# Kernel optimization log

Measured on AMD Instinct MI355X. Metric: run time of the kernel, lower is better.

Reference implementation:

```python
import jax, jax.numpy as jnp
import numpy as np

B, S, D = 16, 512, 2048
NUM_HEADS, NUM_GROUPS = 16, 4
HEAD_DIM = D // NUM_HEADS  # 128
MAX_SEQ_LEN, SHARED_SLOTS = 512, 32
EPS = 1e-6


def _rope_tables(seq_positions):
    # inv_freq over half the head dim, as in the module
    inv_freq = 1.0 / (10000.0 ** (jnp.arange(0, HEAD_DIM, 2, dtype=jnp.float32) / HEAD_DIM))
    freqs = jnp.outer(seq_positions.astype(jnp.float32), inv_freq)  # [S, HEAD_DIM//2]
    return jnp.cos(freqs), jnp.sin(freqs)


def _apply_rope(x, cos, sin):
    # x: [b, s, h, head_dim]; cos/sin: [s, 1, head_dim//2] (broadcast over heads)
    x1, x2 = jnp.split(x, 2, axis=-1)
    real = x1 * cos - x2 * sin
    imag = x1 * sin + x2 * cos
    return jnp.concatenate([real, imag], axis=-1).astype(x.dtype)


def _rmsnorm(x, scale):
    # flax RMSNorm with dtype=float32: compute in fp32
    x = x.astype(jnp.float32)
    ms = jnp.mean(jnp.square(x), axis=-1, keepdims=True)
    return x * jax.lax.rsqrt(ms + EPS) * scale


def setup_inputs() -> dict:
    key = jax.random.key(0)
    ks = jax.random.split(key, 10)
    w = 0.02
    return {
        "x": jax.random.normal(ks[0], (B, S, D), dtype=jnp.float32),
        "wq": jax.random.normal(ks[1], (D, D), dtype=jnp.float32) * w,
        "bq": jnp.zeros((D,), dtype=jnp.float32),
        "wk": jax.random.normal(ks[2], (D, NUM_GROUPS * HEAD_DIM), dtype=jnp.float32) * w,
        "bk": jnp.zeros((NUM_GROUPS * HEAD_DIM,), dtype=jnp.float32),
        "wv": jax.random.normal(ks[3], (D, NUM_GROUPS * HEAD_DIM), dtype=jnp.float32) * w,
        "bv": jnp.zeros((NUM_GROUPS * HEAD_DIM,), dtype=jnp.float32),
        "wo": jax.random.normal(ks[4], (D, D), dtype=jnp.float32) * w,
        "bo": jnp.zeros((D,), dtype=jnp.float32),
        "q_norm_scale": jnp.ones((HEAD_DIM,), dtype=jnp.float32),
        "k_norm_scale": jnp.ones((HEAD_DIM,), dtype=jnp.float32),
    }


def reference(x, wq, bq, wk, bk, wv, bv, wo, bo, q_norm_scale, k_norm_scale):
    b, s, d = x.shape
    rep = NUM_HEADS // NUM_GROUPS
    head_scale = HEAD_DIM ** (-0.5)  # applied once explicitly by the module

    # nnx.Linear(dtype=float16): projections computed in fp16
    xh = x.astype(jnp.float16)
    q = (xh @ wq.astype(jnp.float16) + bq.astype(jnp.float16)).reshape(b, s, NUM_HEADS, HEAD_DIM)
    k = (xh @ wk.astype(jnp.float16) + bk.astype(jnp.float16)).reshape(b, s, NUM_GROUPS, HEAD_DIM)
    v = (xh @ wv.astype(jnp.float16) + bv.astype(jnp.float16)).reshape(b, s, NUM_GROUPS, HEAD_DIM)

    # QK RMSNorm (fp32)
    q = _rmsnorm(q, q_norm_scale)
    k = _rmsnorm(k, k_norm_scale)

    # RoPE (default positions 0..s-1)
    pos = jnp.arange(s)
    cos, sin = _rope_tables(pos)
    cos = cos[:, None, :]
    sin = sin[:, None, :]
    q = _apply_rope(q, cos, sin) * head_scale
    k = _apply_rope(k, cos, sin)

    q = q.astype(jnp.float16)
    k = k.astype(jnp.float16)
    v = v.astype(jnp.float16)

    # GQA without materializing repeated k/v: [b, s, groups, rep, head_dim]
    qg = q.reshape(b, s, NUM_GROUPS, rep, HEAD_DIM)
    # dot_product_attention applies its own 1/sqrt(head_dim) (double-scale, faithful)
    logits = jnp.einsum('btgrh,bsgh->bgrts', qg, k,
                        preferred_element_type=jnp.float32) * head_scale

    causal = pos[:, None] >= pos[None, :]  # [s, s]
    logits = jnp.where(causal[None, None, None, :, :], logits, jnp.finfo(jnp.float32).min)
    probs = jax.nn.softmax(logits, axis=-1).astype(jnp.float16)

    out = jnp.einsum('bgrts,bsgh->btgrh', probs, v)  # [b, s, groups, rep, head_dim]
    out = out.reshape(b, s, d)
    return out @ wo.astype(jnp.float16) + bo.astype(jnp.float16)
```

## Files before the change

kernel.cpp:

```cpp
#include <hip/hip_runtime.h>

#define NB 16
#define NS 512
#define ND 2048
#define NH 16
#define NG 4
#define NHD 128
#define NM (NB * NS)
#define NKD (NG * NHD)
#define NKV 1024
#define HEAD_SCALE 0.08838834764831845f

typedef _Float16 h8 __attribute__((ext_vector_type(8)));
typedef float fx4 __attribute__((ext_vector_type(4)));

__device__ __forceinline__ void gload16(const void* g, void* l) {
  __builtin_amdgcn_global_load_lds(
      (__attribute__((address_space(1))) void*)(unsigned long long)g,
      (__attribute__((address_space(3))) void*)(unsigned long long)l,
      16, 0, 0);
}


__global__ void cvt_x_kernel(const float* __restrict__ in, _Float16* __restrict__ out, int n8) {
  int i = blockIdx.x * 256 + threadIdx.x;
  if (i >= n8) return;
  const fx4* p = (const fx4*)in;
  fx4 a = p[2 * i], b = p[2 * i + 1];
  h8 h;
  h[0] = (_Float16)a[0]; h[1] = (_Float16)a[1]; h[2] = (_Float16)a[2]; h[3] = (_Float16)a[3];
  h[4] = (_Float16)b[0]; h[5] = (_Float16)b[1]; h[6] = (_Float16)b[2]; h[7] = (_Float16)b[3];
  ((h8*)out)[i] = h;
}

__global__ void wtrans_kernel(const float* __restrict__ w, _Float16* __restrict__ wt, int K, int N) {
  __shared__ float t[64][65];
  int n0 = blockIdx.x * 64, k0 = blockIdx.y * 64;
#pragma unroll
  for (int it = 0; it < 16; ++it) {
    int idx = it * 256 + threadIdx.x;
    int r = idx >> 6, c = idx & 63;
    t[r][c] = w[(size_t)(k0 + r) * N + n0 + c];
  }
  __syncthreads();
#pragma unroll
  for (int it = 0; it < 16; ++it) {
    int idx = it * 256 + threadIdx.x;
    int r = idx >> 6, c = idx & 63;
    wt[(size_t)(n0 + r) * K + k0 + c] = (_Float16)t[c][r];
  }
}

__global__ void vtrans_kernel(const _Float16* __restrict__ kv, _Float16* __restrict__ vt) {
  __shared__ _Float16 t[64][72];
  int st = blockIdx.x, dt = blockIdx.y, bg = blockIdx.z;
  int b = bg >> 2, g = bg & 3;
  const _Float16* src = kv + ((size_t)(b * NS + st * 64)) * NKV + NKD + g * NHD + dt * 64;
#pragma unroll
  for (int it = 0; it < 2; ++it) {
    int idx = it * 256 + threadIdx.x;
    int r = idx >> 3, c = (idx & 7) * 8;
    *(h8*)&t[r][c] = *(const h8*)(src + (size_t)r * NKV + c);
  }
  __syncthreads();
  _Float16* dst = vt + ((size_t)bg * NHD + dt * 64) * NS + st * 64;
#pragma unroll
  for (int it = 0; it < 2; ++it) {
    int idx = it * 256 + threadIdx.x;
    int r = idx >> 3, c = (idx & 7) * 8;
    h8 o;
#pragma unroll
    for (int e = 0; e < 8; ++e) o[e] = t[c + e][r];
    *(h8*)(dst + (size_t)r * NS + c) = o;
  }
}

__global__ void rope_tables_kernel(float* __restrict__ cosT, float* __restrict__ sinT) {
  int i = blockIdx.x * 256 + threadIdx.x;
  int s = i >> 6, f = i & 63;
  float inv = exp2f(-(float)f * (13.287712379549449f / 64.0f));
  float a = (float)s * inv;
  cosT[i] = cosf(a);
  sinT[i] = sinf(a);
}

__global__ void norm_rope_kernel(_Float16* __restrict__ X, const float* __restrict__ scale,
                                 const float* __restrict__ cosT, const float* __restrict__ sinT,
                                 int hshift, int rowStride, float outScale) {
  int wid = threadIdx.x >> 6, lane = threadIdx.x & 63;
  int task = blockIdx.x * 4 + wid;
  int row = task >> hshift;
  int head = task & ((1 << hshift) - 1);
  _Float16* p = X + (size_t)row * rowStride + head * NHD;
  float x1 = (float)p[lane], x2 = (float)p[lane + 64];
  float ss = x1 * x1 + x2 * x2;
#pragma unroll
  for (int m = 1; m < 64; m <<= 1) ss += __shfl_xor(ss, m, 64);
  float rn = rsqrtf(ss * (1.0f / 128.0f) + 1e-6f);
  int s = row & (NS - 1);
  float c = cosT[s * 64 + lane], sn = sinT[s * 64 + lane];
  float n1 = x1 * rn * scale[lane], n2 = x2 * rn * scale[64 + lane];
  p[lane] = (_Float16)((n1 * c - n2 * sn) * outScale);
  p[lane + 64] = (_Float16)((n1 * sn + n2 * c) * outScale);
}

__device__ __forceinline__ void st_out(float* p, float v) { *p = v; }
__device__ __forceinline__ void st_out(_Float16* p, float v) { *p = (_Float16)v; }


template <typename OT>
__global__ __launch_bounds__(256, 3) void gemm_bt_kernel(
    const _Float16* __restrict__ A, const _Float16* __restrict__ Bt,
    const float* __restrict__ bias, OT* __restrict__ C, int N, int K) {
  __shared__ alignas(16) _Float16 As[128 * 64];
  __shared__ alignas(16) _Float16 Bs[128 * 64];
  const int tid = threadIdx.x;
  const int lane = tid & 63, wid = tid >> 6;
  const int wr = wid >> 1, wc = wid & 1;
  const int la = lane & 15, lb = (lane >> 4) * 8;
  const int bm = blockIdx.y * 128, bn = blockIdx.x * 128;

  fx4 acc[4][4] = {};

  for (int kt = 0; kt < K; kt += 64) {
    const _Float16* Ag = A + (size_t)bm * K + kt;
    const _Float16* Bg = Bt + (size_t)bn * K + kt;
#pragma unroll
    for (int it = 0; it < 4; ++it) {
      int cb = it * 256 + wid * 64;
      int ca = cb + lane;
      int r = ca >> 3, cc = ca & 7;
      gload16(Ag + (size_t)r * K + cc * 8, &As[cb * 8]);
      gload16(Bg + (size_t)r * K + cc * 8, &Bs[cb * 8]);
    }
    __syncthreads();
#pragma unroll
    for (int kk = 0; kk < 2; ++kk) {
      h8 af[4], bf[4];
#pragma unroll
      for (int m = 0; m < 4; ++m)
        af[m] = *(const h8*)&As[(wr * 64 + m * 16 + la) * 64 + kk * 32 + lb];
#pragma unroll
      for (int n = 0; n < 4; ++n)
        bf[n] = *(const h8*)&Bs[(wc * 64 + n * 16 + la) * 64 + kk * 32 + lb];
#pragma unroll
      for (int m = 0; m < 4; ++m)
#pragma unroll
        for (int n = 0; n < 4; ++n)
          acc[m][n] = __builtin_amdgcn_mfma_f32_16x16x32_f16(af[m], bf[n], acc[m][n], 0, 0, 0);
    }
    __syncthreads();
  }
#pragma unroll
  for (int m = 0; m < 4; ++m) {
    int row0 = bm + wr * 64 + m * 16 + (lane >> 4) * 4;
#pragma unroll
    for (int n = 0; n < 4; ++n) {
      int col = bn + wc * 64 + n * 16 + la;
      float bvv = bias[col];
#pragma unroll
      for (int r = 0; r < 4; ++r)
        st_out(&C[(size_t)(row0 + r) * N + col], acc[m][n][r] + bvv);
    }
  }
}


template <typename OT>
__global__ __launch_bounds__(512, 2) void gemm256_kernel(
    const _Float16* __restrict__ A, const _Float16* __restrict__ Bt,
    const float* __restrict__ bias, OT* __restrict__ C, int N, int K) {
  __shared__ alignas(16) _Float16 As[2][2][256 * 32];
  __shared__ alignas(16) _Float16 Bs[2][2][256 * 32];
  const int tid = threadIdx.x;
  const int lane = tid & 63, w = tid >> 6;
  const int wr = w >> 2, wc = w & 3;
  const int la = lane & 15, lq = lane >> 4;
  const int lin = (blockIdx.x & 7) * 32 + (blockIdx.x >> 3);
  const int nbx = N >> 8;
  const int by = lin / nbx, bx = lin % nbx;
  const int bm = by * 256, bn = bx * 256;
  const int NT = K >> 6;

  fx4 acc[8][4] = {};

  {
    const _Float16* Ag = A + (size_t)bm * K;
    const _Float16* Bg = Bt + (size_t)bn * K;
#pragma unroll
    for (int sh = 0; sh < 2; ++sh) {
#pragma unroll
      for (int i = 0; i < 2; ++i) {
        int cb = i * 512 + w * 64;
        int s = cb + lane;
        int r = s >> 2, c = s & 3;
        gload16(Ag + (size_t)r * K + sh * 32 + ((c ^ ((r >> 1) & 3)) << 3), &As[0][sh][cb * 8]);
      }
#pragma unroll
      for (int i = 0; i < 2; ++i) {
        int cb = i * 512 + w * 64;
        int s = cb + lane;
        int r = s >> 2, c = s & 3;
        gload16(Bg + (size_t)r * K + sh * 32 + ((c ^ ((r >> 1) & 3)) << 3), &Bs[0][sh][cb * 8]);
      }
    }
  }
  asm volatile("s_waitcnt vmcnt(4)" ::: "memory");
  __builtin_amdgcn_s_barrier();

  for (int kt = 0; kt < NT; ++kt) {
    const int cur = kt & 1;
    const int nxt = cur ^ 1;
    const bool more = (kt + 1 < NT);
    const _Float16* Ag = A + (size_t)bm * K + (kt + 1) * 64;
    const _Float16* Bg = Bt + (size_t)bn * K + (kt + 1) * 64;
    h8 bf[4];
#pragma unroll
    for (int ph = 0; ph < 4; ++ph) {
      const int kh = ph >> 1, g = ph & 1;
      h8 af[4];
#pragma unroll
      for (int mi = 0; mi < 4; ++mi) {
        int row = wr * 128 + (g * 4 + mi) * 16 + la;
        af[mi] = *(const h8*)&As[cur][kh][row * 32 + ((lq ^ ((row >> 1) & 3)) << 3)];
      }
      if (g == 0) {
#pragma unroll
        for (int ni = 0; ni < 4; ++ni) {
          int row = wc * 64 + ni * 16 + la;
          bf[ni] = *(const h8*)&Bs[cur][kh][row * 32 + ((lq ^ ((row >> 1) & 3)) << 3)];
        }
      }
      if (more) {
        const int sh = ph >> 1;
        const _Float16* Sg = (ph & 1) ? Bg : Ag;
        _Float16* Ld = (ph & 1) ? &Bs[nxt][sh][0] : &As[nxt][sh][0];
#pragma unroll
        for (int i = 0; i < 2; ++i) {
          int cb = i * 512 + w * 64;
          int s = cb + lane;
          int r = s >> 2, c = s & 3;
          gload16(Sg + (size_t)r * K + sh * 32 + ((c ^ ((r >> 1) & 3)) << 3), Ld + cb * 8);
        }
      }
      if (ph == 1 || ph == 3) {
        if (more) asm volatile("s_waitcnt vmcnt(4)" ::: "memory");
        else      asm volatile("s_waitcnt vmcnt(0)" ::: "memory");
      }
      __builtin_amdgcn_s_barrier();
      asm volatile("s_waitcnt lgkmcnt(0)" ::: "memory");
      __builtin_amdgcn_sched_barrier(0);
      __builtin_amdgcn_s_setprio(1);
#pragma unroll
      for (int mi = 0; mi < 4; ++mi)
#pragma unroll
        for (int ni = 0; ni < 4; ++ni)
          acc[g * 4 + mi][ni] = __builtin_amdgcn_mfma_f32_16x16x32_f16(
              af[mi], bf[ni], acc[g * 4 + mi][ni], 0, 0, 0);
      __builtin_amdgcn_s_setprio(0);
      __builtin_amdgcn_sched_barrier(0);
      __builtin_amdgcn_s_barrier();
    }
  }
#pragma unroll
  for (int mi = 0; mi < 8; ++mi) {
    int row0 = bm + wr * 128 + mi * 16 + lq * 4;
#pragma unroll
    for (int ni = 0; ni < 4; ++ni) {
      int col = bn + wc * 64 + ni * 16 + la;
      float bvv = bias[col];
#pragma unroll
      for (int r = 0; r < 4; ++r)
        st_out(&C[(size_t)(row0 + r) * N + col], acc[mi][ni][r] + bvv);
    }
  }
}


__global__ __launch_bounds__(512, 4) void attn_kernel(
    const _Float16* __restrict__ Q, const _Float16* __restrict__ KV,
    const _Float16* __restrict__ Vt, _Float16* __restrict__ ctx) {
  __shared__ alignas(16) _Float16 Ks[2][64 * 128];
  __shared__ alignas(16) _Float16 Vs[2][128 * 64];
  __shared__ alignas(16) _Float16 Ps[8][16 * 64];

  const int bid = blockIdx.x;
  const int logical = (bid & 7) * 64 + (bid >> 3);
  const int b = logical >> 5;
  const int g = (logical >> 3) & 3;
  const int jp = logical & 7;
  const int j1 = jp, j2 = 15 - jp;

  const int tid = threadIdx.x;
  const int lane = tid & 63, w = tid >> 6;
  const int la = lane & 15, lq = lane >> 4;
  const int h = g * 4 + (w & 3);
  const int rh = w >> 2;

  const _Float16* Vg = Vt + (size_t)(b * NG + g) * NHD * NS;

  auto stage = [&](int buf, int kt) {
    const _Float16* Kg = KV + ((size_t)(b * NS + kt * 64)) * NKV + g * NHD;
#pragma unroll
    for (int it = 0; it < 2; ++it) {
      int cb = it * 512 + w * 64;
      int s = cb + lane;
      int rr = s >> 4, c = s & 15;
      gload16(Kg + (size_t)rr * NKV + ((c ^ (rr & 7)) * 8), &Ks[buf][cb * 8]);
    }
#pragma unroll
    for (int it = 0; it < 2; ++it) {
      int cb = it * 512 + w * 64;
      int s = cb + lane;
      int rr = s >> 3, c = s & 7;
      gload16(Vg + (size_t)rr * NS + kt * 64 + ((c ^ (rr & 7)) * 8), &Vs[buf][cb * 8]);
    }
  };

  const int nt1 = ((j1 * 32 + 31) >> 6) + 1;
  const int nt2 = ((j2 * 32 + 31) >> 6) + 1;
  const int ntotal = nt1 + nt2;

  h8 qf[4];
  fx4 oacc[8];
  float mrun[4], lrun[4];

  stage(0, 0);
  int cur = 0;
  for (int t = 0; t < ntotal; ++t) {
    const bool inA = t < nt1;
    const int j = inA ? j1 : j2;
    const int kt = inA ? t : t - nt1;
    const int ntj = inA ? nt1 : nt2;
    __syncthreads();
    if (t + 1 < ntotal) {
      int nkt = (t + 1 < nt1) ? (t + 1) : (t + 1 - nt1);
      stage(cur ^ 1, nkt);
    }
    if (kt == 0) {
      const _Float16* Qg = Q + ((size_t)(b * NS + j * 32 + rh * 16 + la)) * ND + h * NHD + lq * 8;
#pragma unroll
      for (int kc = 0; kc < 4; ++kc) qf[kc] = *(const h8*)(Qg + kc * 32);
#pragma unroll
      for (int f = 0; f < 8; ++f) oacc[f] = fx4{0.f, 0.f, 0.f, 0.f};
#pragma unroll
      for (int r = 0; r < 4; ++r) { mrun[r] = -1e30f; lrun[r] = 0.f; }
    }

    fx4 sc[4] = {};
    __builtin_amdgcn_s_setprio(1);
#pragma unroll
    for (int n = 0; n < 4; ++n) {
      int row = n * 16 + la;
#pragma unroll
      for (int kc = 0; kc < 4; ++kc) {
        h8 bk = *(const h8*)&Ks[cur][row * 128 + (((kc * 4 + lq) ^ (la & 7)) * 8)];
        sc[n] = __builtin_amdgcn_mfma_f32_16x16x32_f16(qf[kc], bk, sc[n], 0, 0, 0);
      }
    }
    __builtin_amdgcn_s_setprio(0);

    const int qrow0 = j * 32 + rh * 16 + lq * 4;
    const bool maskT = (kt == ntj - 1);
    float pv[4][4];
    float rm[4] = {-1e30f, -1e30f, -1e30f, -1e30f};
#pragma unroll
    for (int n = 0; n < 4; ++n) {
      int kv = kt * 64 + n * 16 + la;
#pragma unroll
      for (int r = 0; r < 4; ++r) {
        float sv = sc[n][r] * HEAD_SCALE;
        sv = (maskT && kv > qrow0 + r) ? -1e30f : sv;
        pv[n][r] = sv;
        rm[r] = fmaxf(rm[r], sv);
      }
    }
#pragma unroll
    for (int r = 0; r < 4; ++r) {
#pragma unroll
      for (int m = 1; m < 16; m <<= 1) rm[r] = fmaxf(rm[r], __shfl_xor(rm[r], m, 64));
      float mn = fmaxf(mrun[r], rm[r]);
      float corr = __expf(mrun[r] - mn);
      mrun[r] = mn;
      lrun[r] *= corr;
#pragma unroll
      for (int f = 0; f < 8; ++f) oacc[f][r] *= corr;
    }
    float rs[4] = {0.f, 0.f, 0.f, 0.f};
#pragma unroll
    for (int n = 0; n < 4; ++n)
#pragma unroll
      for (int r = 0; r < 4; ++r) {
        float e = __expf(pv[n][r] - mrun[r]);
        pv[n][r] = e;
        rs[r] += e;
      }
#pragma unroll
    for (int r = 0; r < 4; ++r) {
#pragma unroll
      for (int m = 1; m < 16; m <<= 1) rs[r] += __shfl_xor(rs[r], m, 64);
      lrun[r] += rs[r];
    }

#pragma unroll
    for (int n = 0; n < 4; ++n)
#pragma unroll
      for (int r = 0; r < 4; ++r) {
        int row = lq * 4 + r;
        int chsw = (n * 2 + (la >> 3)) ^ (row & 7);
        Ps[w][row * 64 + chsw * 8 + (la & 7)] = (_Float16)pv[n][r];
      }
    asm volatile("s_waitcnt lgkmcnt(0)" ::: "memory");
    __builtin_amdgcn_sched_barrier(0);
    h8 pf[2];
#pragma unroll
    for (int ks = 0; ks < 2; ++ks)
      pf[ks] = *(const h8*)&Ps[w][la * 64 + (((ks * 4 + lq) ^ (la & 7)) * 8)];

    __builtin_amdgcn_s_setprio(1);
#pragma unroll
    for (int f = 0; f < 8; ++f) {
      int row = f * 16 + la;
#pragma unroll
      for (int ks = 0; ks < 2; ++ks) {
        h8 bv = *(const h8*)&Vs[cur][row * 64 + (((ks * 4 + lq) ^ (la & 7)) * 8)];
        oacc[f] = __builtin_amdgcn_mfma_f32_16x16x32_f16(pf[ks], bv, oacc[f], 0, 0, 0);
      }
    }
    __builtin_amdgcn_s_setprio(0);

    if (maskT) {
      _Float16* Cg = ctx + ((size_t)(b * NS + qrow0)) * ND + h * NHD + la;
      float inv_l[4];
#pragma unroll
      for (int r = 0; r < 4; ++r) inv_l[r] = 1.0f / lrun[r];
#pragma unroll
      for (int f = 0; f < 8; ++f)
#pragma unroll
        for (int r = 0; r < 4; ++r)
          Cg[(size_t)r * ND + f * 16] = (_Float16)(oacc[f][r] * inv_l[r]);
    }
    cur ^= 1;
  }
}


extern "C" void kernel_launch(void* const* d_in, const int* in_sizes, int n_in,
                              void* d_out, int out_size, void* d_ws, size_t ws_size,
                              hipStream_t stream) {
  (void)in_sizes; (void)n_in; (void)out_size; (void)ws_size;
  const float* x = (const float*)d_in[0];
  const float* wq = (const float*)d_in[1];
  const float* bq = (const float*)d_in[2];
  const float* wk = (const float*)d_in[3];
  const float* bk = (const float*)d_in[4];
  const float* wv = (const float*)d_in[5];
  const float* bv = (const float*)d_in[6];
  const float* wo = (const float*)d_in[7];
  const float* bo = (const float*)d_in[8];
  const float* qns = (const float*)d_in[9];
  const float* kns = (const float*)d_in[10];

  char* ws = (char*)d_ws;
  size_t off = 0;
  _Float16* xh = (_Float16*)(ws + off); off += (size_t)NM * ND * 2;
  _Float16* wqt = (_Float16*)(ws + off); off += (size_t)ND * ND * 2;
  _Float16* wkvt = (_Float16*)(ws + off); off += (size_t)NKV * ND * 2;
  _Float16* wot = (_Float16*)(ws + off); off += (size_t)ND * ND * 2;
  _Float16* Qb = (_Float16*)(ws + off); off += (size_t)NM * ND * 2;
  _Float16* KVbuf = (_Float16*)(ws + off); off += (size_t)NM * NKV * 2;
  float* cosT = (float*)(ws + off); off += (size_t)NS * 64 * 4;
  float* sinT = (float*)(ws + off); off += (size_t)NS * 64 * 4;
  float* bkv = (float*)(ws + off); off += (size_t)NKV * 4;
  _Float16* ctx = xh;
  _Float16* Vtg = wqt;

  cvt_x_kernel<<<NM * ND / 8 / 256, 256, 0, stream>>>(x, xh, NM * ND / 8);
  wtrans_kernel<<<dim3(ND / 64, ND / 64), 256, 0, stream>>>(wq, wqt, ND, ND);
  wtrans_kernel<<<dim3(NKD / 64, ND / 64), 256, 0, stream>>>(wk, wkvt, ND, NKD);
  wtrans_kernel<<<dim3(NKD / 64, ND / 64), 256, 0, stream>>>(wv, wkvt + (size_t)NKD * ND, ND, NKD);
  wtrans_kernel<<<dim3(ND / 64, ND / 64), 256, 0, stream>>>(wo, wot, ND, ND);
  rope_tables_kernel<<<NS * 64 / 256, 256, 0, stream>>>(cosT, sinT);
  hipMemcpyAsync(bkv, bk, NKD * sizeof(float), hipMemcpyDeviceToDevice, stream);
  hipMemcpyAsync(bkv + NKD, bv, NKD * sizeof(float), hipMemcpyDeviceToDevice, stream);

  gemm256_kernel<_Float16><<<dim3(256), dim3(512), 0, stream>>>(xh, wqt, bq, Qb, ND, ND);
  gemm_bt_kernel<_Float16><<<dim3(NKV / 128, NM / 128), 256, 0, stream>>>(xh, wkvt, bkv, KVbuf, NKV, ND);

  norm_rope_kernel<<<NM * NH / 4, 256, 0, stream>>>(Qb, qns, cosT, sinT, 4, ND, HEAD_SCALE);
  norm_rope_kernel<<<NM * NG / 4, 256, 0, stream>>>(KVbuf, kns, cosT, sinT, 2, NKV, 1.0f);

  vtrans_kernel<<<dim3(NS / 64, NHD / 64, NB * NG), 256, 0, stream>>>(KVbuf, Vtg);

  attn_kernel<<<dim3(512), dim3(512), 0, stream>>>(Qb, KVbuf, Vtg, ctx);

  gemm256_kernel<float><<<dim3(256), dim3(512), 0, stream>>>(ctx, wot, bo, (float*)d_out, ND, ND);
}
```

Baseline: 308.5 us.

## Fuse prep kernels into one launch and switch gemm256 to 32x32x16 MFMA

Merges the x conversion, four weight transposes, rope table generation and bias concatenation into a single prep kernel, replacing six launches and two device-to-device memcpys. Separately, the 256x256 GEMM moves from 16x16x32 to 32x32x16 MFMA tiles, with a new LDS swizzle and fragment loads and two phases per k-tile instead of four. The aim is to cut launch overhead and raise MFMA efficiency with fewer LDS reads per FLOP. The trade-off is a different bank-conflict pattern and coarser load/compute interleaving.

Result: slower. 330.8 us (+7.2%).

```diff
diff --git a/kernel.cpp b/kernel.cpp
--- a/kernel.cpp
+++ b/kernel.cpp
@@ -13,6 +13,7 @@
 
 typedef _Float16 h8 __attribute__((ext_vector_type(8)));
 typedef float fx4 __attribute__((ext_vector_type(4)));
+typedef float fx16 __attribute__((ext_vector_type(16)));
 
 __device__ __forceinline__ void gload16(const void* g, void* l) {
   __builtin_amdgcn_global_load_lds(
@@ -22,32 +23,68 @@
 }
 
 
-__global__ void cvt_x_kernel(const float* __restrict__ in, _Float16* __restrict__ out, int n8) {
-  int i = blockIdx.x * 256 + threadIdx.x;
-  if (i >= n8) return;
-  const fx4* p = (const fx4*)in;
-  fx4 a = p[2 * i], b = p[2 * i + 1];
-  h8 h;
-  h[0] = (_Float16)a[0]; h[1] = (_Float16)a[1]; h[2] = (_Float16)a[2]; h[3] = (_Float16)a[3];
-  h[4] = (_Float16)b[0]; h[5] = (_Float16)b[1]; h[6] = (_Float16)b[2]; h[7] = (_Float16)b[3];
-  ((h8*)out)[i] = h;
-}
-
-__global__ void wtrans_kernel(const float* __restrict__ w, _Float16* __restrict__ wt, int K, int N) {
+__global__ void prep_kernel(const float* __restrict__ x, _Float16* __restrict__ xh,
+                            const float* __restrict__ wq, _Float16* __restrict__ wqt,
+                            const float* __restrict__ wk, const float* __restrict__ wv,
+                            _Float16* __restrict__ wkvt,
+                            const float* __restrict__ wo, _Float16* __restrict__ wot,
+                            float* __restrict__ cosT, float* __restrict__ sinT,
+                            const float* __restrict__ bk, const float* __restrict__ bv,
+                            float* __restrict__ bkv) {
   __shared__ float t[64][65];
-  int n0 = blockIdx.x * 64, k0 = blockIdx.y * 64;
+  const int bid = blockIdx.x, tid = threadIdx.x;
+  if (bid < 2048) {
+    const fx4* p = (const fx4*)x;
+    h8* o = (h8*)xh;
+#pragma unroll
+    for (int it = 0; it < 4; ++it) {
+      int i = (it * 2048 + bid) * 256 + tid;
+      fx4 a = p[2 * i], b = p[2 * i + 1];
+      h8 hv;
+      hv[0] = (_Float16)a[0]; hv[1] = (_Float16)a[1]; hv[2] = (_Float16)a[2]; hv[3] = (_Float16)a[3];
+      hv[4] = (_Float16)b[0]; hv[5] = (_Float16)b[1]; hv[6] = (_Float16)b[2]; hv[7] = (_Float16)b[3];
+      o[i] = hv;
+    }
+    return;
+  }
+  int lb = bid - 2048;
+  const float* src;
+  _Float16* dst;
+  int K, N;
+  if (lb < 1024)      { src = wq; dst = wqt; K = ND; N = ND; }
+  else if (lb < 1280) { lb -= 1024; src = wk; dst = wkvt; K = ND; N = NKD; }
+  else if (lb < 1536) { lb -= 1280; src = wv; dst = wkvt + (size_t)NKD * ND; K = ND; N = NKD; }
+  else if (lb < 2560) { lb -= 1536; src = wo; dst = wot; K = ND; N = ND; }
+  else if (lb < 2688) {
+    int i = (lb - 2560) * 256 + tid;
+    int s = i >> 6, f = i & 63;
+    float inv = exp2f(-(float)f * (13.287712379549449f / 64.0f));
+    float a = (float)s * inv;
+    cosT[i] = cosf(a);
+    sinT[i] = sinf(a);
+    return;
+  } else {
+#pragma unroll
+    for (int it = 0; it < 4; ++it) {
+      int idx = it * 256 + tid;
+      bkv[idx] = (idx < NKD) ? bk[idx] : bv[idx - NKD];
+    }
+    return;
+  }
+  const int ntil = N >> 6;
+  const int n0 = (lb % ntil) * 64, k0 = (lb / ntil) * 64;
 #pragma unroll
   for (int it = 0; it < 16; ++it) {
-    int idx = it * 256 + threadIdx.x;
+    int idx = it * 256 + tid;
     int r = idx >> 6, c = idx & 63;
-    t[r][c] = w[(size_t)(k0 + r) * N + n0 + c];
+    t[r][c] = src[(size_t)(k0 + r) * N + n0 + c];
   }
   __syncthreads();
 #pragma unroll
   for (int it = 0; it < 16; ++it) {
-    int idx = it * 256 + threadIdx.x;
+    int idx = it * 256 + tid;
     int r = idx >> 6, c = idx & 63;
-    wt[(size_t)(n0 + r) * K + k0 + c] = (_Float16)t[c][r];
+    dst[(size_t)(n0 + r) * K + k0 + c] = (_Float16)t[c][r];
   }
 }
 
@@ -73,15 +110,6 @@
     for (int e = 0; e < 8; ++e) o[e] = t[c + e][r];
     *(h8*)(dst + (size_t)r * NS + c) = o;
   }
-}
-
-__global__ void rope_tables_kernel(float* __restrict__ cosT, float* __restrict__ sinT) {
-  int i = blockIdx.x * 256 + threadIdx.x;
-  int s = i >> 6, f = i & 63;
-  float inv = exp2f(-(float)f * (13.287712379549449f / 64.0f));
-  float a = (float)s * inv;
-  cosT[i] = cosf(a);
-  sinT[i] = sinf(a);
 }
 
 __global__ void norm_rope_kernel(_Float16* __restrict__ X, const float* __restrict__ scale,
@@ -175,77 +203,64 @@
   const int tid = threadIdx.x;
   const int lane = tid & 63, w = tid >> 6;
   const int wr = w >> 2, wc = w & 3;
-  const int la = lane & 15, lq = lane >> 4;
+  const int l31 = lane & 31, l5 = lane >> 5;
   const int lin = (blockIdx.x & 7) * 32 + (blockIdx.x >> 3);
   const int nbx = N >> 8;
   const int by = lin / nbx, bx = lin % nbx;
   const int bm = by * 256, bn = bx * 256;
   const int NT = K >> 6;
 
-  fx4 acc[8][4] = {};
-
-  {
-    const _Float16* Ag = A + (size_t)bm * K;
-    const _Float16* Bg = Bt + (size_t)bn * K;
-#pragma unroll
-    for (int sh = 0; sh < 2; ++sh) {
-#pragma unroll
-      for (int i = 0; i < 2; ++i) {
-        int cb = i * 512 + w * 64;
-        int s = cb + lane;
-        int r = s >> 2, c = s & 3;
-        gload16(Ag + (size_t)r * K + sh * 32 + ((c ^ ((r >> 1) & 3)) << 3), &As[0][sh][cb * 8]);
-      }
-#pragma unroll
-      for (int i = 0; i < 2; ++i) {
-        int cb = i * 512 + w * 64;
-        int s = cb + lane;
-        int r = s >> 2, c = s & 3;
-        gload16(Bg + (size_t)r * K + sh * 32 + ((c ^ ((r >> 1) & 3)) << 3), &Bs[0][sh][cb * 8]);
-      }
-    }
-  }
+  fx16 acc[4][2] = {};
+
+  auto stage_half = [&](int buf, int kt, int sh, bool aMat) {
+    const _Float16* G = aMat ? (A + (size_t)bm * K + kt * 64)
+                             : (Bt + (size_t)bn * K + kt * 64);
+    _Float16* Ld = aMat ? &As[buf][sh][0] : &Bs[buf][sh][0];
+#pragma unroll
+    for (int i = 0; i < 2; ++i) {
+      int cb = i * 512 + w * 64;
+      int s = cb + lane;
+      int r = s >> 2, c = s & 3;
+      gload16(G + (size_t)r * K + sh * 32 + ((c ^ (r & 3)) << 3), Ld + cb * 8);
+    }
+  };
+
+  stage_half(0, 0, 0, true);
+  stage_half(0, 0, 0, false);
+  stage_half(0, 0, 1, true);
+  stage_half(0, 0, 1, false);
   asm volatile("s_waitcnt vmcnt(4)" ::: "memory");
   __builtin_amdgcn_s_barrier();
 
   for (int kt = 0; kt < NT; ++kt) {
     const int cur = kt & 1;
-    const int nxt = cur ^ 1;
     const bool more = (kt + 1 < NT);
-    const _Float16* Ag = A + (size_t)bm * K + (kt + 1) * 64;
-    const _Float16* Bg = Bt + (size_t)bn * K + (kt + 1) * 64;
-    h8 bf[4];
-#pragma unroll
-    for (int ph = 0; ph < 4; ++ph) {
-      const int kh = ph >> 1, g = ph & 1;
-      h8 af[4];
-#pragma unroll
-      for (int mi = 0; mi < 4; ++mi) {
-        int row = wr * 128 + (g * 4 + mi) * 16 + la;
-        af[mi] = *(const h8*)&As[cur][kh][row * 32 + ((lq ^ ((row >> 1) & 3)) << 3)];
-      }
-      if (g == 0) {
-#pragma unroll
-        for (int ni = 0; ni < 4; ++ni) {
-          int row = wc * 64 + ni * 16 + la;
-          bf[ni] = *(const h8*)&Bs[cur][kh][row * 32 + ((lq ^ ((row >> 1) & 3)) << 3)];
+#pragma unroll
+    for (int ph = 0; ph < 2; ++ph) {
+      const int kh = ph;
+      h8 af[4][2], bf[2][2];
+#pragma unroll
+      for (int mi = 0; mi < 4; ++mi)
+#pragma unroll
+        for (int s = 0; s < 2; ++s) {
+          int row = wr * 128 + mi * 32 + l31;
+          int c = (s * 2 + l5) ^ (row & 3);
+          af[mi][s] = *(const h8*)&As[cur][kh][row * 32 + c * 8];
         }
-      }
+#pragma unroll
+      for (int ni = 0; ni < 2; ++ni)
+#pragma unroll
+        for (int s = 0; s < 2; ++s) {
+          int row = wc * 64 + ni * 32 + l31;
+          int c = (s * 2 + l5) ^ (row & 3);
+          bf[ni][s] = *(const h8*)&Bs[cur][kh][row * 32 + c * 8];
+        }
       if (more) {
-        const int sh = ph >> 1;
-        const _Float16* Sg = (ph & 1) ? Bg : Ag;
-        _Float16* Ld = (ph & 1) ? &Bs[nxt][sh][0] : &As[nxt][sh][0];
-#pragma unroll
-        for (int i = 0; i < 2; ++i) {
-          int cb = i * 512 + w * 64;
-          int s = cb + lane;
-          int r = s >> 2, c = s & 3;
-          gload16(Sg + (size_t)r * K + sh * 32 + ((c ^ ((r >> 1) & 3)) << 3), Ld + cb * 8);
-        }
-      }
-      if (ph == 1 || ph == 3) {
-        if (more) asm volatile("s_waitcnt vmcnt(4)" ::: "memory");
-        else      asm volatile("s_waitcnt vmcnt(0)" ::: "memory");
+        stage_half(cur ^ 1, kt + 1, ph, true);
+        stage_half(cur ^ 1, kt + 1, ph, false);
+        asm volatile("s_waitcnt vmcnt(4)" ::: "memory");
+      } else {
+        asm volatile("s_waitcnt vmcnt(0)" ::: "memory");
       }
       __builtin_amdgcn_s_barrier();
       asm volatile("s_waitcnt lgkmcnt(0)" ::: "memory");
@@ -254,24 +269,28 @@
 #pragma unroll
       for (int mi = 0; mi < 4; ++mi)
 #pragma unroll
-        for (int ni = 0; ni < 4; ++ni)
-          acc[g * 4 + mi][ni] = __builtin_amdgcn_mfma_f32_16x16x32_f16(
-              af[mi], bf[ni], acc[g * 4 + mi][ni], 0, 0, 0);
+        for (int ni = 0; ni < 2; ++ni)
+#pragma unroll
+          for (int s = 0; s < 2; ++s)
+            acc[mi][ni] = __builtin_amdgcn_mfma_f32_32x32x16_f16(
+                af[mi][s], bf[ni][s], acc[mi][ni], 0, 0, 0);
       __builtin_amdgcn_s_setprio(0);
       __builtin_amdgcn_sched_barrier(0);
       __builtin_amdgcn_s_barrier();
     }
   }
 #pragma unroll
-  for (int mi = 0; mi < 8; ++mi) {
-    int row0 = bm + wr * 128 + mi * 16 + lq * 4;
-#pragma unroll
-    for (int ni = 0; ni < 4; ++ni) {
-      int col = bn + wc * 64 + ni * 16 + la;
+  for (int mi = 0; mi < 4; ++mi) {
+#pragma unroll
+    for (int ni = 0; ni < 2; ++ni) {
+      int col = bn + wc * 64 + ni * 32 + l31;
       float bvv = bias[col];
-#pragma unroll
-      for (int r = 0; r < 4; ++r)
-        st_out(&C[(size_t)(row0 + r) * N + col], acc[mi][ni][r] + bvv);
+      int rbase = bm + wr * 128 + mi * 32 + 4 * l5;
+#pragma unroll
+      for (int reg = 0; reg < 16; ++reg) {
+        int row = rbase + (reg & 3) + 8 * (reg >> 2);
+        st_out(&C[(size_t)row * N + col], acc[mi][ni][reg] + bvv);
+      }
     }
   }
 }
@@ -475,14 +494,8 @@
   _Float16* ctx = xh;
   _Float16* Vtg = wqt;
 
-  cvt_x_kernel<<<NM * ND / 8 / 256, 256, 0, stream>>>(x, xh, NM * ND / 8);
-  wtrans_kernel<<<dim3(ND / 64, ND / 64), 256, 0, stream>>>(wq, wqt, ND, ND);
-  wtrans_kernel<<<dim3(NKD / 64, ND / 64), 256, 0, stream>>>(wk, wkvt, ND, NKD);
-  wtrans_kernel<<<dim3(NKD / 64, ND / 64), 256, 0, stream>>>(wv, wkvt + (size_t)NKD * ND, ND, NKD);
-  wtrans_kernel<<<dim3(ND / 64, ND / 64), 256, 0, stream>>>(wo, wot, ND, ND);
-  rope_tables_kernel<<<NS * 64 / 256, 256, 0, stream>>>(cosT, sinT);
-  hipMemcpyAsync(bkv, bk, NKD * sizeof(float), hipMemcpyDeviceToDevice, stream);
-  hipMemcpyAsync(bkv + NKD, bv, NKD * sizeof(float), hipMemcpyDeviceToDevice, stream);
+  prep_kernel<<<dim3(4737), 256, 0, stream>>>(x, xh, wq, wqt, wk, wv, wkvt, wo, wot,
+                                              cosT, sinT, bk, bv, bkv);
 
   gemm256_kernel<_Float16><<<dim3(256), dim3(512), 0, stream>>>(xh, wqt, bq, Qb, ND, ND);
   gemm_bt_kernel<_Float16><<<dim3(NKV / 128, NM / 128), 256, 0, stream>>>(xh, wkvt, bkv, KVbuf, NKV, ND);
```

## Merge prep kernels, merge Q/K norm-rope launches, preload Q fragments in attention

Applied to the files above, without the earlier changes.

Folds the x conversion, four weight transposes, RoPE table generation and the bias copies into one prep kernel, and merges the two norm/RoPE launches into one grid. This cuts launch count and lets small jobs share the GPU. In the attention kernel, both query tiles' fragments are loaded before the loop. The per-iteration __syncthreads is replaced by an explicit vmcnt wait plus s_barrier, so the next tile's prefetch can stay in flight. Risks are higher register pressure from holding two Q fragment sets, and a wait count that must exactly match the number of loads issued by stage.

New measurement: 334.7 us. 8.5% more time.

```diff
diff --git a/kernel.cpp b/kernel.cpp
--- a/kernel.cpp
+++ b/kernel.cpp
@@ -22,32 +22,68 @@
 }
 
 
-__global__ void cvt_x_kernel(const float* __restrict__ in, _Float16* __restrict__ out, int n8) {
-  int i = blockIdx.x * 256 + threadIdx.x;
-  if (i >= n8) return;
-  const fx4* p = (const fx4*)in;
-  fx4 a = p[2 * i], b = p[2 * i + 1];
-  h8 h;
-  h[0] = (_Float16)a[0]; h[1] = (_Float16)a[1]; h[2] = (_Float16)a[2]; h[3] = (_Float16)a[3];
-  h[4] = (_Float16)b[0]; h[5] = (_Float16)b[1]; h[6] = (_Float16)b[2]; h[7] = (_Float16)b[3];
-  ((h8*)out)[i] = h;
-}
-
-__global__ void wtrans_kernel(const float* __restrict__ w, _Float16* __restrict__ wt, int K, int N) {
+__global__ void prep_kernel(const float* __restrict__ x, _Float16* __restrict__ xh,
+                            const float* __restrict__ wq, _Float16* __restrict__ wqt,
+                            const float* __restrict__ wk, const float* __restrict__ wv,
+                            _Float16* __restrict__ wkvt,
+                            const float* __restrict__ wo, _Float16* __restrict__ wot,
+                            float* __restrict__ cosT, float* __restrict__ sinT,
+                            const float* __restrict__ bk, const float* __restrict__ bv,
+                            float* __restrict__ bkv) {
   __shared__ float t[64][65];
-  int n0 = blockIdx.x * 64, k0 = blockIdx.y * 64;
+  const int bid = blockIdx.x, tid = threadIdx.x;
+  if (bid < 2048) {
+    const fx4* p = (const fx4*)x;
+    h8* o = (h8*)xh;
+#pragma unroll
+    for (int it = 0; it < 4; ++it) {
+      int i = (it * 2048 + bid) * 256 + tid;
+      fx4 a = p[2 * i], b = p[2 * i + 1];
+      h8 hv;
+      hv[0] = (_Float16)a[0]; hv[1] = (_Float16)a[1]; hv[2] = (_Float16)a[2]; hv[3] = (_Float16)a[3];
+      hv[4] = (_Float16)b[0]; hv[5] = (_Float16)b[1]; hv[6] = (_Float16)b[2]; hv[7] = (_Float16)b[3];
+      o[i] = hv;
+    }
+    return;
+  }
+  int lb = bid - 2048;
+  const float* src;
+  _Float16* dst;
+  int K, N;
+  if (lb < 1024)      { src = wq; dst = wqt; K = ND; N = ND; }
+  else if (lb < 1280) { lb -= 1024; src = wk; dst = wkvt; K = ND; N = NKD; }
+  else if (lb < 1536) { lb -= 1280; src = wv; dst = wkvt + (size_t)NKD * ND; K = ND; N = NKD; }
+  else if (lb < 2560) { lb -= 1536; src = wo; dst = wot; K = ND; N = ND; }
+  else if (lb < 2688) {
+    int i = (lb - 2560) * 256 + tid;
+    int s = i >> 6, f = i & 63;
+    float inv = exp2f(-(float)f * (13.287712379549449f / 64.0f));
+    float a = (float)s * inv;
+    cosT[i] = cosf(a);
+    sinT[i] = sinf(a);
+    return;
+  } else {
+#pragma unroll
+    for (int it = 0; it < 4; ++it) {
+      int idx = it * 256 + tid;
+      bkv[idx] = (idx < NKD) ? bk[idx] : bv[idx - NKD];
+    }
+    return;
+  }
+  const int ntil = N >> 6;
+  const int n0 = (lb % ntil) * 64, k0 = (lb / ntil) * 64;
 #pragma unroll
   for (int it = 0; it < 16; ++it) {
-    int idx = it * 256 + threadIdx.x;
+    int idx = it * 256 + tid;
     int r = idx >> 6, c = idx & 63;
-    t[r][c] = w[(size_t)(k0 + r) * N + n0 + c];
+    t[r][c] = src[(size_t)(k0 + r) * N + n0 + c];
   }
   __syncthreads();
 #pragma unroll
   for (int it = 0; it < 16; ++it) {
-    int idx = it * 256 + threadIdx.x;
+    int idx = it * 256 + tid;
     int r = idx >> 6, c = idx & 63;
-    wt[(size_t)(n0 + r) * K + k0 + c] = (_Float16)t[c][r];
+    dst[(size_t)(n0 + r) * K + k0 + c] = (_Float16)t[c][r];
   }
 }
 
@@ -75,20 +111,18 @@
   }
 }
 
-__global__ void rope_tables_kernel(float* __restrict__ cosT, float* __restrict__ sinT) {
-  int i = blockIdx.x * 256 + threadIdx.x;
-  int s = i >> 6, f = i & 63;
-  float inv = exp2f(-(float)f * (13.287712379549449f / 64.0f));
-  float a = (float)s * inv;
-  cosT[i] = cosf(a);
-  sinT[i] = sinf(a);
-}
-
-__global__ void norm_rope_kernel(_Float16* __restrict__ X, const float* __restrict__ scale,
-                                 const float* __restrict__ cosT, const float* __restrict__ sinT,
-                                 int hshift, int rowStride, float outScale) {
+__global__ void norm_rope_kernel(_Float16* __restrict__ Qb, _Float16* __restrict__ KVb,
+                                 const float* __restrict__ qns, const float* __restrict__ kns,
+                                 const float* __restrict__ cosT, const float* __restrict__ sinT) {
+  int bid = blockIdx.x;
+  _Float16* X;
+  const float* scale;
+  int hshift, rowStride;
+  float outScale;
+  if (bid < 32768) { X = Qb; scale = qns; hshift = 4; rowStride = ND; outScale = HEAD_SCALE; }
+  else { bid -= 32768; X = KVb; scale = kns; hshift = 2; rowStride = NKV; outScale = 1.0f; }
   int wid = threadIdx.x >> 6, lane = threadIdx.x & 63;
-  int task = blockIdx.x * 4 + wid;
+  int task = bid * 4 + wid;
   int row = task >> hshift;
   int head = task & ((1 << hshift) - 1);
   _Float16* p = X + (size_t)row * rowStride + head * NHD;
@@ -321,26 +355,37 @@
   const int nt2 = ((j2 * 32 + 31) >> 6) + 1;
   const int ntotal = nt1 + nt2;
 
-  h8 qf[4];
+  stage(0, 0);
+  h8 qfA[4], qfB[4];
+  {
+    const _Float16* QgA = Q + ((size_t)(b * NS + j1 * 32 + rh * 16 + la)) * ND + h * NHD + lq * 8;
+    const _Float16* QgB = Q + ((size_t)(b * NS + j2 * 32 + rh * 16 + la)) * ND + h * NHD + lq * 8;
+#pragma unroll
+    for (int kc = 0; kc < 4; ++kc) {
+      qfA[kc] = *(const h8*)(QgA + kc * 32);
+      qfB[kc] = *(const h8*)(QgB + kc * 32);
+    }
+  }
+
   fx4 oacc[8];
   float mrun[4], lrun[4];
 
-  stage(0, 0);
   int cur = 0;
   for (int t = 0; t < ntotal; ++t) {
     const bool inA = t < nt1;
     const int j = inA ? j1 : j2;
     const int kt = inA ? t : t - nt1;
     const int ntj = inA ? nt1 : nt2;
-    __syncthreads();
-    if (t + 1 < ntotal) {
+    const bool more = (t + 1 < ntotal);
+    if (more) {
       int nkt = (t + 1 < nt1) ? (t + 1) : (t + 1 - nt1);
       stage(cur ^ 1, nkt);
-    }
+      asm volatile("s_waitcnt vmcnt(4)" ::: "memory");
+    } else {
+      asm volatile("s_waitcnt vmcnt(0)" ::: "memory");
+    }
+    __builtin_amdgcn_s_barrier();
     if (kt == 0) {
-      const _Float16* Qg = Q + ((size_t)(b * NS + j * 32 + rh * 16 + la)) * ND + h * NHD + lq * 8;
-#pragma unroll
-      for (int kc = 0; kc < 4; ++kc) qf[kc] = *(const h8*)(Qg + kc * 32);
 #pragma unroll
       for (int f = 0; f < 8; ++f) oacc[f] = fx4{0.f, 0.f, 0.f, 0.f};
 #pragma unroll
@@ -354,8 +399,9 @@
       int row = n * 16 + la;
 #pragma unroll
       for (int kc = 0; kc < 4; ++kc) {
+        h8 qv = inA ? qfA[kc] : qfB[kc];
         h8 bk = *(const h8*)&Ks[cur][row * 128 + (((kc * 4 + lq) ^ (la & 7)) * 8)];
-        sc[n] = __builtin_amdgcn_mfma_f32_16x16x32_f16(qf[kc], bk, sc[n], 0, 0, 0);
+        sc[n] = __builtin_amdgcn_mfma_f32_16x16x32_f16(qv, bk, sc[n], 0, 0, 0);
       }
     }
     __builtin_amdgcn_s_setprio(0);
@@ -475,20 +521,13 @@
   _Float16* ctx = xh;
   _Float16* Vtg = wqt;
 
-  cvt_x_kernel<<<NM * ND / 8 / 256, 256, 0, stream>>>(x, xh, NM * ND / 8);
-  wtrans_kernel<<<dim3(ND / 64, ND / 64), 256, 0, stream>>>(wq, wqt, ND, ND);
-  wtrans_kernel<<<dim3(NKD / 64, ND / 64), 256, 0, stream>>>(wk, wkvt, ND, NKD);
-  wtrans_kernel<<<dim3(NKD / 64, ND / 64), 256, 0, stream>>>(wv, wkvt + (size_t)NKD * ND, ND, NKD);
-  wtrans_kernel<<<dim3(ND / 64, ND / 64), 256, 0, stream>>>(wo, wot, ND, ND);
-  rope_tables_kernel<<<NS * 64 / 256, 256, 0, stream>>>(cosT, sinT);
-  hipMemcpyAsync(bkv, bk, NKD * sizeof(float), hipMemcpyDeviceToDevice, stream);
-  hipMemcpyAsync(bkv + NKD, bv, NKD * sizeof(float), hipMemcpyDeviceToDevice, stream);
+  prep_kernel<<<dim3(4737), 256, 0, stream>>>(x, xh, wq, wqt, wk, wv, wkvt, wo, wot,
+                                              cosT, sinT, bk, bv, bkv);
 
   gemm256_kernel<_Float16><<<dim3(256), dim3(512), 0, stream>>>(xh, wqt, bq, Qb, ND, ND);
   gemm_bt_kernel<_Float16><<<dim3(NKV / 128, NM / 128), 256, 0, stream>>>(xh, wkvt, bkv, KVbuf, NKV, ND);
 
-  norm_rope_kernel<<<NM * NH / 4, 256, 0, stream>>>(Qb, qns, cosT, sinT, 4, ND, HEAD_SCALE);
-  norm_rope_kernel<<<NM * NG / 4, 256, 0, stream>>>(KVbuf, kns, cosT, sinT, 2, NKV, 1.0f);
+  norm_rope_kernel<<<dim3(40960), 256, 0, stream>>>(Qb, KVbuf, qns, kns, cosT, sinT);
 
   vtrans_kernel<<<dim3(NS / 64, NHD / 64, NB * NG), 256, 0, stream>>>(KVbuf, Vtg);
 
```
